# Performance work log

Measured on AMD Instinct MI355X. Metric: run time of the kernel, lower is better.

Reference implementation:

```python
import jax, jax.numpy as jnp
import numpy as np
from itertools import product

EPS = 1e-6
P = 3  # heatmap_size; corr channels = P**3 = 27


def l2_on_axis(x, axis=1):
    return jnp.sqrt(jnp.sum(x * x, axis=axis, keepdims=True) + EPS)


def reduce_masked_mean(x, mask):
    return jnp.sum(x * mask) / (jnp.sum(mask) + EPS)


def smoothl1(d):
    a = jnp.abs(d)
    return jnp.where(a < 1.0, 0.5 * d * d, a - 0.5)


def corr3d(f0, f1):
    # 3D correlation volume, patch P^3, zero padding. (B,C,D,H,W)->(B,P^3,D,H,W)
    B, C, D, H, W = f0.shape
    pad = P // 2
    f1p = jnp.pad(f1, ((0, 0), (0, 0), (pad, pad), (pad, pad), (pad, pad)))
    outs = []
    for dz in range(P):
        for dy in range(P):
            for dx in range(P):
                s = f1p[:, :, dz:dz + D, dy:dy + H, dx:dx + W]
                outs.append(jnp.einsum('bcdhw,bcdhw->bdhw', f0, s))
    return jnp.stack(outs, axis=1)


def flow_head(cc, W1, b1, W2, b2):
    cc = jax.nn.relu(cc)
    cc = cc / (jnp.sqrt(jnp.sum(cc * cc, axis=1, keepdims=True)) + EPS)  # l2_normalize dim=1
    h = jnp.einsum('oc,bcdhw->bodhw', W1, cc) + b1[None, :, None, None, None]
    h = jnp.where(h > 0, h, 0.01 * h)  # LeakyReLU
    return jnp.einsum('oc,bcdhw->bodhw', W2, h) + b2[None, :, None, None, None]


def backwarp(feat, flow):
    # trilinear backwarp, zero padding outside; flow ch: (dx->W, dy->H, dz->D)
    B, C, D, H, W = feat.shape
    zz, yy, xx = jnp.meshgrid(jnp.arange(D, dtype=flow.dtype),
                              jnp.arange(H, dtype=flow.dtype),
                              jnp.arange(W, dtype=flow.dtype), indexing='ij')
    xs = xx[None] + flow[:, 0]
    ys = yy[None] + flow[:, 1]
    zs = zz[None] + flow[:, 2]
    x0, y0, z0 = jnp.floor(xs), jnp.floor(ys), jnp.floor(zs)
    featf = feat.reshape(B, C, D * H * W)
    out = jnp.zeros_like(feat)
    for cz, cy, cx in product((0, 1), (0, 1), (0, 1)):
        zi, yi, xi = z0 + cz, y0 + cy, x0 + cx
        w = (1 - jnp.abs(zs - zi)) * (1 - jnp.abs(ys - yi)) * (1 - jnp.abs(xs - xi))
        valid = ((zi >= 0) & (zi < D) & (yi >= 0) & (yi < H) & (xi >= 0) & (xi < W)).astype(feat.dtype)
        idx = ((jnp.clip(zi, 0, D - 1) * H + jnp.clip(yi, 0, H - 1)) * W
               + jnp.clip(xi, 0, W - 1)).astype(jnp.int32).reshape(B, -1)
        g = jnp.take_along_axis(featf, idx[:, None, :], axis=2).reshape(B, C, D, H, W)
        out = out + g * (w * valid)[:, None]
    return out


def gradient3d_abs(x):
    dz = jnp.abs(jnp.pad(x[:, :, 1:] - x[:, :, :-1], ((0, 0), (0, 0), (0, 1), (0, 0), (0, 0))))
    dy = jnp.abs(jnp.pad(x[:, :, :, 1:] - x[:, :, :, :-1], ((0, 0), (0, 0), (0, 0), (0, 1), (0, 0))))
    dx = jnp.abs(jnp.pad(x[:, :, :, :, 1:] - x[:, :, :, :, :-1], ((0, 0), (0, 0), (0, 0), (0, 0), (0, 1))))
    return dx, dy, dz


def setup_inputs() -> dict:
    key = jax.random.key(0)
    ks = jax.random.split(key, 8)
    B, C, D, H, W = 2, 32, 64, 64, 64
    return {
        'feat0': jax.random.normal(ks[0], (B, C, D, H, W), jnp.float32),
        'feat1': jax.random.normal(ks[1], (B, C, D, H, W), jnp.float32),
        'flow_g': jax.random.normal(ks[2], (B, 3, D, H, W), jnp.float32),
        'mask_g': jax.random.uniform(ks[3], (B, 1, D, H, W), jnp.float32),
        'W1': jax.random.normal(ks[4], (64, P ** 3), jnp.float32) * 0.05,
        'b1': jnp.zeros((64,), jnp.float32),
        'W2': jax.random.normal(ks[5], (3, 64), jnp.float32) * 0.05,
        'b2': jnp.zeros((3,), jnp.float32),
        'is_synth': 0,
    }


def reference(feat0, feat1, flow_g, mask_g, W1, b1, W2, b2, is_synth):
    B, C, D, H, W = feat0.shape
    # hinge loss (feat1_aligned == feat1 at iteration 0)
    hinge_vox = jax.nn.relu(0.2 - l2_on_axis(feat1 - feat0))
    hinge_mask = (jnp.sum(jnp.abs(flow_g), axis=1, keepdims=True) > 1.0).astype(feat0.dtype)
    hinge_loss = reduce_masked_mean(hinge_vox, hinge_mask)

    # single scale sc=1.0
    flow_forw = flow_head(corr3d(feat0, feat1), W1, b1, W2, b2)
    flow_back = flow_head(corr3d(feat1, feat0), W1, b1, W2, b2)

    feat1_aligned = backwarp(feat1, flow_forw)
    ones1 = jnp.ones((B, 1, D, H, W), feat0.dtype)
    valid1 = backwarp(ones1, flow_forw)
    valid0 = backwarp(ones1, flow_forw)  # faithful: source also uses flow_total_forw

    feat_diff = reduce_masked_mean(l2_on_axis(feat1_aligned - feat0), valid1 * valid0)
    warp_loss_cumu = feat_diff  # * sc (=1)

    l1_diff = jnp.mean(smoothl1(flow_forw - flow_g), axis=1, keepdims=True)
    l2_diff = jnp.mean((flow_forw - flow_g) ** 2, axis=1, keepdims=True)
    nonzero = (jnp.sum(jnp.abs(flow_g), axis=1, keepdims=True) > 0.01).astype(feat0.dtype) * mask_g
    yeszero = (1.0 - nonzero) * mask_g
    l1_bal = 0.5 * (reduce_masked_mean(l1_diff, nonzero) + reduce_masked_mean(l1_diff, yeszero))
    l2_bal = 0.5 * (reduce_masked_mean(l2_diff, nonzero) + reduce_masked_mean(l2_diff, yeszero))

    fb_al = backwarp(flow_back, jax.lax.stop_gradient(flow_forw))
    ff_al = backwarp(flow_forw, jax.lax.stop_gradient(flow_back))
    cycle_loss = jnp.mean(smoothl1(flow_forw + fb_al)) + jnp.mean(smoothl1(flow_back + ff_al))

    dx, dy, dz = gradient3d_abs(flow_forw)
    smooth_forw = jnp.mean(dx + dy + dx, axis=1, keepdims=True)  # faithful: dx counted twice
    dx, dy, dz = gradient3d_abs(flow_back)
    smooth_back = jnp.mean(dx + dy + dx, axis=1, keepdims=True)
    smooth_loss = jnp.mean((smooth_forw + smooth_back) * 0.5)

    # all hyp coefficients = 1.0; is_synth selects identical coeffs here
    total_loss = hinge_loss + cycle_loss + l1_bal + l2_bal + warp_loss_cumu + smooth_loss
    return total_loss, flow_forw
```

## Files before the change

kernel.cpp:

```cpp
#include <hip/hip_runtime.h>
#include <math.h>

#define EPSF 1e-6f

typedef __attribute__((ext_vector_type(8))) short short8;
typedef __attribute__((ext_vector_type(4))) float f32x4;

constexpr int Bn = 2, Cn = 32, Dn = 64, Hn = 64, Wn = 64;
constexpr int HW  = Hn * Wn;
constexpr int DHW = Dn * HW;
constexpr int NVOX = Bn * DHW;


__device__ inline float sl1(float d) {
    float a = fabsf(d);
    return a < 1.f ? 0.5f * d * d : a - 0.5f;
}

__device__ inline int xcd_swz(int bid) {
    return (bid & 7) * 256 + (bid >> 3);
}

__device__ inline float dpp_left(float v) {
    int r = __builtin_amdgcn_update_dpp(0, __float_as_int(v), 0x138 ,
                                        0xF, 0xF, true);
    return __int_as_float(r);
}
__device__ inline float dpp_right(float v) {
    int r = __builtin_amdgcn_update_dpp(0, __float_as_int(v), 0x130 ,
                                        0xF, 0xF, true);
    return __int_as_float(r);
}

__device__ inline unsigned int bf16b(float f) {
    return (__float_as_uint(f) + 0x8000u) >> 16;
}
__device__ inline unsigned int bfpack(float lo, float hi) {
    return bf16b(lo) | ((__float_as_uint(hi) + 0x8000u) & 0xffff0000u);
}
__device__ inline float bf2f(unsigned short u) {
    return __uint_as_float((unsigned int)u << 16);
}

struct PairGather {
    int   pidx[4];
    int   sel[4];
    float w0[4], w1[4];
};

__device__ inline void warp_pair_setup(float flx, float fly, float flz,
                                       int x, int y, int z,
                                       PairGather& pg, float& wsum) {
    float xs = (float)x + flx, ys = (float)y + fly, zs = (float)z + flz;
    float xf = floorf(xs), yf = floorf(ys), zf = floorf(zs);
    float fx = xs - xf, fy = ys - yf, fz = zs - zf;
    int xi = (int)xf, yi = (int)yf, zi = (int)zf;

    int x0c = min(max(xi, 0), Wn - 1);
    bool xv0 = (xi >= 0) && (xi < Wn);
    bool xv1 = (xi + 1 >= 0) && (xi + 1 < Wn);
    int sel = (xi >= 0 && xi < Wn - 1) ? 1 : 0;
    float wx0 = xv0 ? (1.f - fx) : 0.f;
    float wx1 = xv1 ? fx : 0.f;

    wsum = 0.f;
#pragma unroll
    for (int cz = 0; cz < 2; cz++) {
        int zz = zi + cz;
        bool zv = (zz >= 0) && (zz < Dn);
        int zc = min(max(zz, 0), Dn - 1);
        float wz = (cz ? fz : 1.f - fz) * (zv ? 1.f : 0.f);
#pragma unroll
        for (int cy = 0; cy < 2; cy++) {
            int yy = yi + cy;
            bool yv = (yy >= 0) && (yy < Hn);
            int yc = min(max(yy, 0), Hn - 1);
            float wy = (cy ? fy : 1.f - fy) * (yv ? 1.f : 0.f);
            int k = cz * 2 + cy;
            int sp = (zc * Hn + yc) * Wn + x0c;
            pg.pidx[k] = min(sp, DHW - 2);
            pg.sel[k] = sel;
            float wzy = wz * wy;
            pg.w0[k] = wzy * wx0;
            pg.w1[k] = wzy * wx1;
            wsum += pg.w0[k] + pg.w1[k];
        }
    }
}

__device__ inline float gather8(const float* __restrict__ slab, const PairGather& pg) {
    float g = 0.f;
#pragma unroll
    for (int k = 0; k < 4; k++) {
        float2 v = *reinterpret_cast<const float2*>(slab + pg.pidx[k]);
        float second = pg.sel[k] ? v.y : v.x;
        g = fmaf(v.x, pg.w0[k], g);
        g = fmaf(second, pg.w1[k], g);
    }
    return g;
}

__global__ void prep_kernel(const float* __restrict__ W1, ushort* __restrict__ W1bf) {
    int i = blockIdx.x * 256 + threadIdx.x;
    if (i < 64 * 32) {
        int n = i >> 5, k = i & 31;
        float val = (k < 27) ? W1[n * 27 + k] : 0.f;
        W1bf[n * 40 + k] = (ushort)bf16b(val);
    }
}

__device__ __forceinline__ void flow_head_mfma(
        float* acc, ushort (&ccS)[4][64][40], int wid, int lane,
        const ushort* __restrict__ W1bf, const float* __restrict__ b1,
        const float* __restrict__ W2, const float* __restrict__ b2,
        float* __restrict__ flow_out, size_t fb0,
        float& mfx, float& mfy, float& mfz) {
    float ss = 0.f;
#pragma unroll
    for (int i = 0; i < 27; i++) {
        float r = acc[i] > 0.f ? acc[i] : 0.f;
        acc[i] = r;
        ss = fmaf(r, r, ss);
    }
    float inv = 1.0f / (sqrtf(ss) + EPSF);
#pragma unroll
    for (int i = 0; i < 27; i++) acc[i] *= inv;

    {
        unsigned int pk[16];
#pragma unroll
        for (int i = 0; i < 13; i++) pk[i] = bfpack(acc[2 * i], acc[2 * i + 1]);
        pk[13] = bfpack(acc[26], 0.f);
        pk[14] = 0u; pk[15] = 0u;
        uint2* rowp = reinterpret_cast<uint2*>(&ccS[wid][lane][0]);
#pragma unroll
        for (int i = 0; i < 8; i++) rowp[i] = make_uint2(pk[2 * i], pk[2 * i + 1]);
    }

    int c0 = lane & 15, oct = lane >> 4;

    short8 bfr[4];
#pragma unroll
    for (int t = 0; t < 4; t++)
        bfr[t] = *reinterpret_cast<const short8*>(W1bf + (size_t)(t * 16 + c0) * 40 + oct * 8);

    f32x4 b1v[4], w2f0[4], w2f1[4], w2f2[4];
#pragma unroll
    for (int mt = 0; mt < 4; mt++) {
        b1v[mt]  = *reinterpret_cast<const f32x4*>(b1 + mt * 16 + oct * 4);
        w2f0[mt] = *reinterpret_cast<const f32x4*>(W2 + mt * 16 + oct * 4);
        w2f1[mt] = *reinterpret_cast<const f32x4*>(W2 + 64 + mt * 16 + oct * 4);
        w2f2[mt] = *reinterpret_cast<const f32x4*>(W2 + 128 + mt * 16 + oct * 4);
    }
    float bb0 = b2[0], bb1 = b2[1], bb2 = b2[2];

#pragma unroll
    for (int nt = 0; nt < 4; nt++) {
        short8 afr = *reinterpret_cast<const short8*>(&ccS[wid][nt * 16 + c0][oct * 8]);
        f32x4 ac[4];
#pragma unroll
        for (int mt = 0; mt < 4; mt++) {
            f32x4 zero = {0.f, 0.f, 0.f, 0.f};
            ac[mt] = __builtin_amdgcn_mfma_f32_16x16x32_bf16(bfr[mt], afr, zero, 0, 0, 0);
        }
        float p0 = 0.f, p1 = 0.f, p2 = 0.f;
#pragma unroll
        for (int mt = 0; mt < 4; mt++) {
#pragma unroll
            for (int rg = 0; rg < 4; rg++) {
                float h = ac[mt][rg] + b1v[mt][rg];
                h = fmaxf(h, 0.01f * h);
                p0 = fmaf(w2f0[mt][rg], h, p0);
                p1 = fmaf(w2f1[mt][rg], h, p1);
                p2 = fmaf(w2f2[mt][rg], h, p2);
            }
        }
        p0 += __shfl_xor(p0, 16); p0 += __shfl_xor(p0, 32);
        p1 += __shfl_xor(p1, 16); p1 += __shfl_xor(p1, 32);
        p2 += __shfl_xor(p2, 16); p2 += __shfl_xor(p2, 32);
        if (oct == nt) {
            int vox = nt * 16 + c0;
            mfx = p0 + bb0; mfy = p1 + bb1; mfz = p2 + bb2;
            flow_out[fb0 + vox]           = mfx;
            flow_out[fb0 + DHW + vox]     = mfy;
            flow_out[fb0 + 2 * DHW + vox] = mfz;
        }
    }
}

__global__ __launch_bounds__(256)
void corr_fwd_kernel(const float* __restrict__ feat0, const float* __restrict__ feat1,
                     const ushort* __restrict__ W1bf, const float* __restrict__ b1,
                     const float* __restrict__ W2, const float* __restrict__ b2,
                     float* __restrict__ flow_forw,
                     const float* __restrict__ flow_g, const float* __restrict__ mask_g,
                     float* __restrict__ accum, ushort* __restrict__ craw) {
    __shared__ ushort ccS[4][64][40];

    int tid = threadIdx.x;
    int lane = tid & 63;
    int wid = __builtin_amdgcn_readfirstlane(tid >> 6);

    int R = xcd_swz(blockIdx.x) * 4 + wid;
    int y = R & 63, z = (R >> 6) & 63, b = R >> 12;

    const float* rp[9];
    float rmask[9];
    {
        int idx = 0;
#pragma unroll
        for (int dz = -1; dz <= 1; dz++) {
#pragma unroll
            for (int dy = -1; dy <= 1; dy++, idx++) {
                int zz = z + dz, yy = y + dy;
                bool valid = (zz >= 0) && (zz < Dn) && (yy >= 0) && (yy < Hn);
                int zc = min(max(zz, 0), Dn - 1);
                int yc = min(max(yy, 0), Hn - 1);
                rp[idx] = feat1 + (size_t)b * Cn * DHW + (size_t)zc * HW + (size_t)yc * Wn;
                rmask[idx] = valid ? 1.f : 0.f;
            }
        }
    }
    const float* ap = feat0 + (size_t)b * Cn * DHW + (size_t)z * HW + (size_t)y * Wn;

    float C[9], TL[9], TR[9];
#pragma unroll
    for (int r = 0; r < 9; r++) { C[r] = 0.f; TL[r] = 0.f; TR[r] = 0.f; }
    float diff2 = 0.f;

#pragma unroll 2
    for (int c = 0; c < Cn; c++) {
        float a = ap[lane];
        float rowv[9];
#pragma unroll
        for (int r = 0; r < 9; r++) rowv[r] = rp[r][lane];
        ap += DHW;
#pragma unroll
        for (int r = 0; r < 9; r++) rp[r] += DHW;

        float aL = dpp_left(a);
        float aR = dpp_right(a);
        float d = rowv[4] - a;
        diff2 = fmaf(d, d, diff2);
#pragma unroll
        for (int r = 0; r < 9; r++) {
            float rv = rowv[r];
            C[r]  = fmaf(a,  rv, C[r]);
            TL[r] = fmaf(aL, rv, TL[r]);
            TR[r] = fmaf(aR, rv, TR[r]);
        }
    }

    float acc[27];
#pragma unroll
    for (int r = 0; r < 9; r++) {
        acc[r * 3 + 0] = dpp_left(TR[r]) * rmask[r];
        acc[r * 3 + 1] = C[r] * rmask[r];
        acc[r * 3 + 2] = dpp_right(TL[r]) * rmask[r];
    }

    size_t vidx = (size_t)R * 64 + lane;
#pragma unroll
    for (int i = 0; i < 27; i++)
        craw[(size_t)i * NVOX + vidx] = (ushort)bf16b(acc[i]);

    size_t fb0 = (size_t)b * 3 * DHW + (size_t)z * HW + (size_t)y * Wn;
    float mfx, mfy, mfz;
    flow_head_mfma(acc, ccS, wid, lane, W1bf, b1, W2, b2, flow_forw, fb0,
                   mfx, mfy, mfz);

    size_t fbase = fb0 + lane;
    float gx = flow_g[fbase], gy = flow_g[fbase + DHW], gz = flow_g[fbase + 2 * DHW];
    float mg = mask_g[(size_t)b * DHW + (size_t)z * HW + y * Wn + lane];

    float ag = fabsf(gx) + fabsf(gy) + fabsf(gz);
    float hmask = ag > 1.0f ? 1.f : 0.f;
    float hv = 0.2f - sqrtf(diff2 + EPSF);
    hv = hv > 0.f ? hv : 0.f;

    float dx0 = mfx - gx, dy0 = mfy - gy, dz0 = mfz - gz;
    float l1 = (sl1(dx0) + sl1(dy0) + sl1(dz0)) * (1.f / 3.f);
    float l2 = (dx0 * dx0 + dy0 * dy0 + dz0 * dz0) * (1.f / 3.f);
    float nz = (ag > 0.01f ? 1.f : 0.f) * mg;
    float yz = (1.f - nz) * mg;

    PairGather pgF; float wsum;
    warp_pair_setup(mfx, mfy, mfz, lane, y, z, pgF, wsum);
    const float* f1b = feat1 + (size_t)b * Cn * DHW;
    const float* f0c = feat0 + (size_t)b * Cn * DHW + (size_t)z * HW + y * Wn + lane;
    float s = 0.f;
#pragma unroll 4
    for (int c = 0; c < Cn; c++) {
        float g = gather8(f1b + (size_t)c * DHW, pgF);
        float d = g - f0c[(size_t)c * DHW];
        s = fmaf(d, d, s);
    }
    float vm = wsum * wsum;
    float wnum = sqrtf(s + EPSF) * vm;

    float pv[10];
    pv[0] = hv * hmask; pv[1] = hmask;
    pv[2] = wnum;       pv[3] = vm;
    pv[4] = l1 * nz;    pv[5] = l1 * yz;
    pv[6] = l2 * nz;    pv[7] = l2 * yz;
    pv[8] = nz;         pv[9] = yz;

#pragma unroll
    for (int i = 0; i < 10; i++) {
        float val = pv[i];
        for (int off = 32; off; off >>= 1) val += __shfl_down(val, off, 64);
        pv[i] = val;
    }
    __shared__ float sred[10][4];
    if (lane == 0) {
#pragma unroll
        for (int i = 0; i < 10; i++) sred[i][wid] = pv[i];
    }
    __syncthreads();
    if (tid < 10) {
        atomicAdd(&accum[tid], sred[tid][0] + sred[tid][1] + sred[tid][2] + sred[tid][3]);
    }
}

__global__ __launch_bounds__(256)
void corr_bwd_kernel(const ushort* __restrict__ craw,
                     const ushort* __restrict__ W1bf, const float* __restrict__ b1,
                     const float* __restrict__ W2, const float* __restrict__ b2,
                     float* __restrict__ flow_back) {
    __shared__ ushort ccS[4][64][40];

    int tid = threadIdx.x;
    int lane = tid & 63;
    int wid = __builtin_amdgcn_readfirstlane(tid >> 6);

    int R = xcd_swz(blockIdx.x) * 4 + wid;
    int y = R & 63, z = (R >> 6) & 63, b = R >> 12;

    float acc[27];
#pragma unroll
    for (int sz = 0; sz < 3; sz++) {
#pragma unroll
        for (int sy = 0; sy < 3; sy++) {
            int zz = z + sz - 1, yy = y + sy - 1;
            bool valid = (zz >= 0) && (zz < Dn) && (yy >= 0) && (yy < Hn);
            int zc = min(max(zz, 0), Dn - 1);
            int yc = min(max(yy, 0), Hn - 1);
            float m = valid ? 1.f : 0.f;
            const ushort* rowb = craw + (size_t)b * DHW + (size_t)zc * HW + (size_t)yc * Wn + lane;
            int base = (sz * 3 + sy) * 3;
            float v0 = bf2f(rowb[(size_t)(26 - base) * NVOX]);
            float v1 = bf2f(rowb[(size_t)(25 - base) * NVOX]);
            float v2 = bf2f(rowb[(size_t)(24 - base) * NVOX]);
            acc[base + 0] = dpp_left(v0) * m;
            acc[base + 1] = v1 * m;
            acc[base + 2] = dpp_right(v2) * m;
        }
    }

    size_t fb0 = (size_t)b * 3 * DHW + (size_t)z * HW + (size_t)y * Wn;
    float mfx, mfy, mfz;
    flow_head_mfma(acc, ccS, wid, lane, W1bf, b1, W2, b2, flow_back, fb0,
                   mfx, mfy, mfz);
}

__global__ __launch_bounds__(256)
void slim_loss_kernel(const float* __restrict__ flowf, const float* __restrict__ flowb,
                      float* __restrict__ accum) {
    int tid = threadIdx.x;
    int v = xcd_swz(blockIdx.x) * 256 + tid;
    int x = v & 63, y = (v >> 6) & 63, z = (v >> 12) & 63, b = v >> 18;

    size_t sp = (size_t)z * HW + y * Wn + x;
    size_t f3 = (size_t)b * 3 * DHW + sp;

    float ffx = flowf[f3], ffy = flowf[f3 + DHW], ffz = flowf[f3 + 2 * DHW];
    float fbx = flowb[f3], fby = flowb[f3 + DHW], fbz = flowb[f3 + 2 * DHW];

    PairGather pgF; float wsumF;
    warp_pair_setup(ffx, ffy, ffz, x, y, z, pgF, wsumF);
    const float* fb_b = flowb + (size_t)b * 3 * DHW;
    float fbalx = gather8(fb_b, pgF);
    float fbaly = gather8(fb_b + DHW, pgF);
    float fbalz = gather8(fb_b + 2 * DHW, pgF);
    float cyc1 = sl1(ffx + fbalx) + sl1(ffy + fbaly) + sl1(ffz + fbalz);

    PairGather pgB; float wsumB;
    warp_pair_setup(fbx, fby, fbz, x, y, z, pgB, wsumB);
    const float* ff_b = flowf + (size_t)b * 3 * DHW;
    float ffalx = gather8(ff_b, pgB);
    float ffaly = gather8(ff_b + DHW, pgB);
    float ffalz = gather8(ff_b + 2 * DHW, pgB);
    float cyc2 = sl1(fbx + ffalx) + sl1(fby + ffaly) + sl1(fbz + ffalz);

    float sf = 0.f, sb2v = 0.f;
#pragma unroll
    for (int j = 0; j < 3; j++) {
        const float* pf = flowf + f3 + (size_t)j * DHW;
        float c0 = pf[0];
        float ddx = (x < Wn - 1) ? fabsf(pf[1] - c0) : 0.f;
        float ddy = (y < Hn - 1) ? fabsf(pf[Wn] - c0) : 0.f;
        sf += 2.f * ddx + ddy;
        const float* pb = flowb + f3 + (size_t)j * DHW;
        float c1 = pb[0];
        float ddx2 = (x < Wn - 1) ? fabsf(pb[1] - c1) : 0.f;
        float ddy2 = (y < Hn - 1) ? fabsf(pb[Wn] - c1) : 0.f;
        sb2v += 2.f * ddx2 + ddy2;
    }
    float smoothv = 0.5f * (sf * (1.f / 3.f) + sb2v * (1.f / 3.f));

    float pv[3] = { cyc1, cyc2, smoothv };
#pragma unroll
    for (int i = 0; i < 3; i++) {
        float val = pv[i];
        for (int off = 32; off; off >>= 1) val += __shfl_down(val, off, 64);
        pv[i] = val;
    }
    __shared__ float sred[3][4];
    int lane = tid & 63, wid = tid >> 6;
    if (lane == 0) {
#pragma unroll
        for (int i = 0; i < 3; i++) sred[i][wid] = pv[i];
    }
    __syncthreads();
    if (tid < 3) {
        atomicAdd(&accum[10 + tid], sred[tid][0] + sred[tid][1] + sred[tid][2] + sred[tid][3]);
    }
}

__global__ void finalize_kernel(const float* __restrict__ accum, float* __restrict__ out) {
    float hinge = accum[0] / (accum[1] + EPSF);
    float warp  = accum[2] / (accum[3] + EPSF);
    float l1b = 0.5f * (accum[4] / (accum[8] + EPSF) + accum[5] / (accum[9] + EPSF));
    float l2b = 0.5f * (accum[6] / (accum[8] + EPSF) + accum[7] / (accum[9] + EPSF));
    float n3 = 3.0f * (float)NVOX;
    float cyc = accum[10] / n3 + accum[11] / n3;
    float sm  = accum[12] / (float)NVOX;
    out[0] = hinge + cyc + l1b + l2b + warp + sm;
}

extern "C" void kernel_launch(void* const* d_in, const int* in_sizes, int n_in,
                              void* d_out, int out_size, void* d_ws, size_t ws_size,
                              hipStream_t stream) {
    const float* feat0  = (const float*)d_in[0];
    const float* feat1  = (const float*)d_in[1];
    const float* flow_g = (const float*)d_in[2];
    const float* mask_g = (const float*)d_in[3];
    const float* W1     = (const float*)d_in[4];
    const float* b1     = (const float*)d_in[5];
    const float* W2     = (const float*)d_in[6];
    const float* b2     = (const float*)d_in[7];

    float* out = (float*)d_out;
    float* accum = (float*)d_ws;
    ushort* W1bf = (ushort*)((char*)d_ws + 128);
    const size_t FLOWB_OFF = 8192;
    const size_t FLOWB_BYTES = (size_t)Bn * 3 * DHW * sizeof(float);
    float* flow_back = (float*)((char*)d_ws + FLOWB_OFF);
    const size_t CRAW_OFF = FLOWB_OFF + FLOWB_BYTES;
    ushort* craw = (ushort*)((char*)d_ws + CRAW_OFF);
    float* flow_forw = out + 1;

    hipMemsetAsync(d_ws, 0, 64, stream);

    dim3 block(256);
    prep_kernel<<<dim3(8), block, 0, stream>>>(W1, W1bf);

    corr_fwd_kernel<<<dim3(NVOX / 256), block, 0, stream>>>(
        feat0, feat1, W1bf, b1, W2, b2, flow_forw, flow_g, mask_g, accum, craw);
    corr_bwd_kernel<<<dim3(NVOX / 256), block, 0, stream>>>(
        craw, W1bf, b1, W2, b2, flow_back);
    slim_loss_kernel<<<dim3(NVOX / 256), block, 0, stream>>>(flow_forw, flow_back, accum);
    finalize_kernel<<<1, 1, 0, stream>>>(accum, out);
}
```

Measured before the change: 164.8 us.

## Process both batch elements per wave in forward correlation kernel

Each wave in the forward correlation kernel now handles the same (z,y) row for both batch items. It keeps two sets of 27 accumulators, runs the flow head twice, and does the warp-loss gathers for both batches in one loop. The grid is halved and the XCD swizzle chunk is adjusted to match. The aim is more independent loads and FMAs in flight per wave, plus shared address setup and fewer reductions and atomics. The cost is roughly twice the register use, which can lower occupancy or cause spills, and half as many blocks to fill the GPU.

```diff
diff --git a/kernel.cpp b/kernel.cpp
--- a/kernel.cpp
+++ b/kernel.cpp
@@ -10,6 +10,7 @@
 constexpr int HW  = Hn * Wn;
 constexpr int DHW = Dn * HW;
 constexpr int NVOX = Bn * DHW;
+constexpr size_t BS = (size_t)Cn * DHW;
 
 
 __device__ inline float sl1(float d) {
@@ -17,8 +18,8 @@
     return a < 1.f ? 0.5f * d * d : a - 0.5f;
 }
 
-__device__ inline int xcd_swz(int bid) {
-    return (bid & 7) * 256 + (bid >> 3);
+__device__ inline int xcd_swz(int bid, int chunk) {
+    return (bid & 7) * chunk + (bid >> 3);
 }
 
 __device__ inline float dpp_left(float v) {
@@ -201,10 +202,10 @@
     int lane = tid & 63;
     int wid = __builtin_amdgcn_readfirstlane(tid >> 6);
 
-    int R = xcd_swz(blockIdx.x) * 4 + wid;
-    int y = R & 63, z = (R >> 6) & 63, b = R >> 12;
-
-    const float* rp[9];
+    int R = xcd_swz(blockIdx.x, 128) * 4 + wid;
+    int y = R & 63, z = R >> 6;
+
+    const float* rp0[9];
     float rmask[9];
     {
         int idx = 0;
@@ -216,94 +217,124 @@
                 bool valid = (zz >= 0) && (zz < Dn) && (yy >= 0) && (yy < Hn);
                 int zc = min(max(zz, 0), Dn - 1);
                 int yc = min(max(yy, 0), Hn - 1);
-                rp[idx] = feat1 + (size_t)b * Cn * DHW + (size_t)zc * HW + (size_t)yc * Wn;
+                rp0[idx] = feat1 + (size_t)zc * HW + (size_t)yc * Wn;
                 rmask[idx] = valid ? 1.f : 0.f;
             }
         }
     }
-    const float* ap = feat0 + (size_t)b * Cn * DHW + (size_t)z * HW + (size_t)y * Wn;
-
-    float C[9], TL[9], TR[9];
-#pragma unroll
-    for (int r = 0; r < 9; r++) { C[r] = 0.f; TL[r] = 0.f; TR[r] = 0.f; }
-    float diff2 = 0.f;
+    const float* ap0 = feat0 + (size_t)z * HW + (size_t)y * Wn;
+
+    float C0[9], TL0[9], TR0[9], C1[9], TL1[9], TR1[9];
+#pragma unroll
+    for (int r = 0; r < 9; r++) {
+        C0[r] = 0.f; TL0[r] = 0.f; TR0[r] = 0.f;
+        C1[r] = 0.f; TL1[r] = 0.f; TR1[r] = 0.f;
+    }
+    float diff2_0 = 0.f, diff2_1 = 0.f;
 
 #pragma unroll 2
     for (int c = 0; c < Cn; c++) {
-        float a = ap[lane];
-        float rowv[9];
-#pragma unroll
-        for (int r = 0; r < 9; r++) rowv[r] = rp[r][lane];
-        ap += DHW;
-#pragma unroll
-        for (int r = 0; r < 9; r++) rp[r] += DHW;
-
-        float aL = dpp_left(a);
-        float aR = dpp_right(a);
-        float d = rowv[4] - a;
-        diff2 = fmaf(d, d, diff2);
+        float a0 = ap0[lane];
+        float a1 = ap0[lane + BS];
+        float rv0[9], rv1[9];
 #pragma unroll
         for (int r = 0; r < 9; r++) {
-            float rv = rowv[r];
-            C[r]  = fmaf(a,  rv, C[r]);
-            TL[r] = fmaf(aL, rv, TL[r]);
-            TR[r] = fmaf(aR, rv, TR[r]);
-        }
-    }
-
-    float acc[27];
-#pragma unroll
-    for (int r = 0; r < 9; r++) {
-        acc[r * 3 + 0] = dpp_left(TR[r]) * rmask[r];
-        acc[r * 3 + 1] = C[r] * rmask[r];
-        acc[r * 3 + 2] = dpp_right(TL[r]) * rmask[r];
-    }
-
-    size_t vidx = (size_t)R * 64 + lane;
-#pragma unroll
-    for (int i = 0; i < 27; i++)
-        craw[(size_t)i * NVOX + vidx] = (ushort)bf16b(acc[i]);
-
-    size_t fb0 = (size_t)b * 3 * DHW + (size_t)z * HW + (size_t)y * Wn;
-    float mfx, mfy, mfz;
-    flow_head_mfma(acc, ccS, wid, lane, W1bf, b1, W2, b2, flow_forw, fb0,
-                   mfx, mfy, mfz);
-
-    size_t fbase = fb0 + lane;
-    float gx = flow_g[fbase], gy = flow_g[fbase + DHW], gz = flow_g[fbase + 2 * DHW];
-    float mg = mask_g[(size_t)b * DHW + (size_t)z * HW + y * Wn + lane];
-
-    float ag = fabsf(gx) + fabsf(gy) + fabsf(gz);
-    float hmask = ag > 1.0f ? 1.f : 0.f;
-    float hv = 0.2f - sqrtf(diff2 + EPSF);
-    hv = hv > 0.f ? hv : 0.f;
-
-    float dx0 = mfx - gx, dy0 = mfy - gy, dz0 = mfz - gz;
-    float l1 = (sl1(dx0) + sl1(dy0) + sl1(dz0)) * (1.f / 3.f);
-    float l2 = (dx0 * dx0 + dy0 * dy0 + dz0 * dz0) * (1.f / 3.f);
-    float nz = (ag > 0.01f ? 1.f : 0.f) * mg;
-    float yz = (1.f - nz) * mg;
-
-    PairGather pgF; float wsum;
-    warp_pair_setup(mfx, mfy, mfz, lane, y, z, pgF, wsum);
-    const float* f1b = feat1 + (size_t)b * Cn * DHW;
-    const float* f0c = feat0 + (size_t)b * Cn * DHW + (size_t)z * HW + y * Wn + lane;
-    float s = 0.f;
+            rv0[r] = rp0[r][lane];
+            rv1[r] = rp0[r][lane + BS];
+        }
+        ap0 += DHW;
+#pragma unroll
+        for (int r = 0; r < 9; r++) rp0[r] += DHW;
+
+        float aL0 = dpp_left(a0), aR0 = dpp_right(a0);
+        float aL1 = dpp_left(a1), aR1 = dpp_right(a1);
+        float d0 = rv0[4] - a0; diff2_0 = fmaf(d0, d0, diff2_0);
+        float d1 = rv1[4] - a1; diff2_1 = fmaf(d1, d1, diff2_1);
+#pragma unroll
+        for (int r = 0; r < 9; r++) {
+            float v0 = rv0[r], v1 = rv1[r];
+            C0[r]  = fmaf(a0,  v0, C0[r]);
+            TL0[r] = fmaf(aL0, v0, TL0[r]);
+            TR0[r] = fmaf(aR0, v0, TR0[r]);
+            C1[r]  = fmaf(a1,  v1, C1[r]);
+            TL1[r] = fmaf(aL1, v1, TL1[r]);
+            TR1[r] = fmaf(aR1, v1, TR1[r]);
+        }
+    }
+
+    float mf[2][3];
+    float pv[10];
+#pragma unroll
+    for (int i = 0; i < 10; i++) pv[i] = 0.f;
+
+#pragma unroll
+    for (int j = 0; j < 2; j++) {
+        float acc[27];
+#pragma unroll
+        for (int r = 0; r < 9; r++) {
+            float m = rmask[r];
+            if (j == 0) {
+                acc[r * 3 + 0] = dpp_left(TR0[r]) * m;
+                acc[r * 3 + 1] = C0[r] * m;
+                acc[r * 3 + 2] = dpp_right(TL0[r]) * m;
+            } else {
+                acc[r * 3 + 0] = dpp_left(TR1[r]) * m;
+                acc[r * 3 + 1] = C1[r] * m;
+                acc[r * 3 + 2] = dpp_right(TL1[r]) * m;
+            }
+        }
+
+        size_t vidx = (size_t)(R + j * 4096) * 64 + lane;
+#pragma unroll
+        for (int i = 0; i < 27; i++)
+            craw[(size_t)i * NVOX + vidx] = (ushort)bf16b(acc[i]);
+
+        size_t fb0 = (size_t)j * 3 * DHW + (size_t)z * HW + (size_t)y * Wn;
+        flow_head_mfma(acc, ccS, wid, lane, W1bf, b1, W2, b2, flow_forw, fb0,
+                       mf[j][0], mf[j][1], mf[j][2]);
+
+        size_t fbase = fb0 + lane;
+        float gx = flow_g[fbase], gy = flow_g[fbase + DHW], gz = flow_g[fbase + 2 * DHW];
+        float mg = mask_g[(size_t)j * DHW + (size_t)z * HW + (size_t)y * Wn + lane];
+
+        float ag = fabsf(gx) + fabsf(gy) + fabsf(gz);
+        float hmask = ag > 1.0f ? 1.f : 0.f;
+        float dd2 = j == 0 ? diff2_0 : diff2_1;
+        float hv = 0.2f - sqrtf(dd2 + EPSF);
+        hv = hv > 0.f ? hv : 0.f;
+
+        float dx0 = mf[j][0] - gx, dy0 = mf[j][1] - gy, dz0 = mf[j][2] - gz;
+        float l1 = (sl1(dx0) + sl1(dy0) + sl1(dz0)) * (1.f / 3.f);
+        float l2 = (dx0 * dx0 + dy0 * dy0 + dz0 * dz0) * (1.f / 3.f);
+        float nz = (ag > 0.01f ? 1.f : 0.f) * mg;
+        float yz = (1.f - nz) * mg;
+
+        pv[0] += hv * hmask; pv[1] += hmask;
+        pv[4] += l1 * nz;    pv[5] += l1 * yz;
+        pv[6] += l2 * nz;    pv[7] += l2 * yz;
+        pv[8] += nz;         pv[9] += yz;
+    }
+
+    {
+        PairGather pg0, pg1; float ws0, ws1;
+        warp_pair_setup(mf[0][0], mf[0][1], mf[0][2], lane, y, z, pg0, ws0);
+        warp_pair_setup(mf[1][0], mf[1][1], mf[1][2], lane, y, z, pg1, ws1);
+        const float* f1b0 = feat1;
+        const float* f0c0 = feat0 + (size_t)z * HW + (size_t)y * Wn + lane;
+        float s0 = 0.f, s1 = 0.f;
 #pragma unroll 4
-    for (int c = 0; c < Cn; c++) {
-        float g = gather8(f1b + (size_t)c * DHW, pgF);
-        float d = g - f0c[(size_t)c * DHW];
-        s = fmaf(d, d, s);
-    }
-    float vm = wsum * wsum;
-    float wnum = sqrtf(s + EPSF) * vm;
-
-    float pv[10];
-    pv[0] = hv * hmask; pv[1] = hmask;
-    pv[2] = wnum;       pv[3] = vm;
-    pv[4] = l1 * nz;    pv[5] = l1 * yz;
-    pv[6] = l2 * nz;    pv[7] = l2 * yz;
-    pv[8] = nz;         pv[9] = yz;
+        for (int c = 0; c < Cn; c++) {
+            float g0 = gather8(f1b0 + (size_t)c * DHW, pg0);
+            float g1 = gather8(f1b0 + BS + (size_t)c * DHW, pg1);
+            float d0 = g0 - f0c0[(size_t)c * DHW];
+            float d1 = g1 - f0c0[BS + (size_t)c * DHW];
+            s0 = fmaf(d0, d0, s0);
+            s1 = fmaf(d1, d1, s1);
+        }
+        float vm0 = ws0 * ws0, vm1 = ws1 * ws1;
+        pv[2] = sqrtf(s0 + EPSF) * vm0 + sqrtf(s1 + EPSF) * vm1;
+        pv[3] = vm0 + vm1;
+    }
 
 #pragma unroll
     for (int i = 0; i < 10; i++) {
@@ -333,7 +364,7 @@
     int lane = tid & 63;
     int wid = __builtin_amdgcn_readfirstlane(tid >> 6);
 
-    int R = xcd_swz(blockIdx.x) * 4 + wid;
+    int R = xcd_swz(blockIdx.x, 256) * 4 + wid;
     int y = R & 63, z = (R >> 6) & 63, b = R >> 12;
 
     float acc[27];
@@ -367,7 +398,7 @@
 void slim_loss_kernel(const float* __restrict__ flowf, const float* __restrict__ flowb,
                       float* __restrict__ accum) {
     int tid = threadIdx.x;
-    int v = xcd_swz(blockIdx.x) * 256 + tid;
+    int v = xcd_swz(blockIdx.x, 256) * 256 + tid;
     int x = v & 63, y = (v >> 6) & 63, z = (v >> 12) & 63, b = v >> 18;
 
     size_t sp = (size_t)z * HW + y * Wn + x;
@@ -465,7 +496,7 @@
     dim3 block(256);
     prep_kernel<<<dim3(8), block, 0, stream>>>(W1, W1bf);
 
-    corr_fwd_kernel<<<dim3(NVOX / 256), block, 0, stream>>>(
+    corr_fwd_kernel<<<dim3(NVOX / 512), block, 0, stream>>>(
         feat0, feat1, W1bf, b1, W2, b2, flow_forw, flow_g, mask_g, accum, craw);
     corr_bwd_kernel<<<dim3(NVOX / 256), block, 0, stream>>>(
         craw, W1bf, b1, W2, b2, flow_back);
```

New measurement: 163.5 us. Within noise of the previous version (-0.8%).

## Stage shared feat1 neighbor rows in LDS with double buffering across waves

Applied to the files above, without the earlier changes.

The four waves in a block cover four consecutive y rows, and their 3x3 neighborhoods overlap. The correlation kernel now loads the 18 distinct feat1 rows per channel cooperatively into double-buffered LDS, prefetching the next channel into registers while the current one is computed. Each wave then reads its 9 rows from LDS instead of issuing 9 global loads per channel, cutting redundant global and cache traffic. The cost is a block-wide barrier every channel iteration, the LDS buffer being aliased with the flow-head staging area, and the loop no longer being unrolled.

```diff
diff --git a/kernel.cpp b/kernel.cpp
--- a/kernel.cpp
+++ b/kernel.cpp
@@ -10,6 +10,7 @@
 constexpr int HW  = Hn * Wn;
 constexpr int DHW = Dn * HW;
 constexpr int NVOX = Bn * DHW;
+constexpr size_t BS = (size_t)Cn * DHW;
 
 
 __device__ inline float sl1(float d) {
@@ -17,8 +18,8 @@
     return a < 1.f ? 0.5f * d * d : a - 0.5f;
 }
 
-__device__ inline int xcd_swz(int bid) {
-    return (bid & 7) * 256 + (bid >> 3);
+__device__ inline int xcd_swz(int bid, int chunk) {
+    return (bid & 7) * chunk + (bid >> 3);
 }
 
 __device__ inline float dpp_left(float v) {
@@ -110,7 +111,7 @@
 }
 
 __device__ __forceinline__ void flow_head_mfma(
-        float* acc, ushort (&ccS)[4][64][40], int wid, int lane,
+        float* acc, ushort (*ccS)[64][40], int wid, int lane,
         const ushort* __restrict__ W1bf, const float* __restrict__ b1,
         const float* __restrict__ W2, const float* __restrict__ b2,
         float* __restrict__ flow_out, size_t fb0,
@@ -195,16 +196,18 @@
                      float* __restrict__ flow_forw,
                      const float* __restrict__ flow_g, const float* __restrict__ mask_g,
                      float* __restrict__ accum, ushort* __restrict__ craw) {
-    __shared__ ushort ccS[4][64][40];
+    __shared__ __align__(16) char smem[4 * 64 * 40 * 2];
+    float (*sfeat)[18][64] = reinterpret_cast<float(*)[18][64]>(smem);
+    ushort (*ccS)[64][40]  = reinterpret_cast<ushort(*)[64][40]>(smem);
 
     int tid = threadIdx.x;
     int lane = tid & 63;
     int wid = __builtin_amdgcn_readfirstlane(tid >> 6);
 
-    int R = xcd_swz(blockIdx.x) * 4 + wid;
+    int R = xcd_swz(blockIdx.x, 256) * 4 + wid;
     int y = R & 63, z = (R >> 6) & 63, b = R >> 12;
-
-    const float* rp[9];
+    int y0 = y & ~3;
+
     float rmask[9];
     {
         int idx = 0;
@@ -213,33 +216,60 @@
 #pragma unroll
             for (int dy = -1; dy <= 1; dy++, idx++) {
                 int zz = z + dz, yy = y + dy;
-                bool valid = (zz >= 0) && (zz < Dn) && (yy >= 0) && (yy < Hn);
-                int zc = min(max(zz, 0), Dn - 1);
-                int yc = min(max(yy, 0), Hn - 1);
-                rp[idx] = feat1 + (size_t)b * Cn * DHW + (size_t)zc * HW + (size_t)yc * Wn;
-                rmask[idx] = valid ? 1.f : 0.f;
+                rmask[idx] = ((zz >= 0) && (zz < Dn) && (yy >= 0) && (yy < Hn)) ? 1.f : 0.f;
             }
         }
     }
-    const float* ap = feat0 + (size_t)b * Cn * DHW + (size_t)z * HW + (size_t)y * Wn;
+
+    const float* srp[5];
+#pragma unroll
+    for (int p = 0; p < 5; p++) {
+        int row = p * 4 + wid;
+        if (row < 18) {
+            int zc = min(max(z + row / 6 - 1, 0), Dn - 1);
+            int yc = min(max(y0 + row % 6 - 1, 0), Hn - 1);
+            srp[p] = feat1 + (size_t)b * BS + (size_t)zc * HW + (size_t)yc * Wn;
+        } else srp[p] = feat1;
+    }
+    const float* ap = feat0 + (size_t)b * BS + (size_t)z * HW + (size_t)y * Wn;
 
     float C[9], TL[9], TR[9];
 #pragma unroll
     for (int r = 0; r < 9; r++) { C[r] = 0.f; TL[r] = 0.f; TR[r] = 0.f; }
     float diff2 = 0.f;
 
-#pragma unroll 2
+#pragma unroll
+    for (int p = 0; p < 5; p++)
+        if (p * 4 + wid < 18)
+            sfeat[0][p * 4 + wid][lane] = srp[p][lane];
+    __syncthreads();
+
+#pragma unroll 1
     for (int c = 0; c < Cn; c++) {
+        int buf = c & 1;
         float a = ap[lane];
+        ap += DHW;
+
+        float stg[5];
+        if (c + 1 < Cn) {
+#pragma unroll
+            for (int p = 0; p < 5; p++)
+                if (p * 4 + wid < 18) { srp[p] += DHW; stg[p] = srp[p][lane]; }
+        }
+
         float rowv[9];
 #pragma unroll
-        for (int r = 0; r < 9; r++) rowv[r] = rp[r][lane];
-        ap += DHW;
-#pragma unroll
-        for (int r = 0; r < 9; r++) rp[r] += DHW;
-
-        float aL = dpp_left(a);
-        float aR = dpp_right(a);
+        for (int r = 0; r < 9; r++)
+            rowv[r] = sfeat[buf][(r / 3) * 6 + wid + (r % 3)][lane];
+
+        if (c + 1 < Cn) {
+#pragma unroll
+            for (int p = 0; p < 5; p++)
+                if (p * 4 + wid < 18)
+                    sfeat[buf ^ 1][p * 4 + wid][lane] = stg[p];
+        }
+
+        float aL = dpp_left(a), aR = dpp_right(a);
         float d = rowv[4] - a;
         diff2 = fmaf(d, d, diff2);
 #pragma unroll
@@ -249,6 +279,7 @@
             TL[r] = fmaf(aL, rv, TL[r]);
             TR[r] = fmaf(aR, rv, TR[r]);
         }
+        __syncthreads();
     }
 
     float acc[27];
@@ -286,8 +317,8 @@
 
     PairGather pgF; float wsum;
     warp_pair_setup(mfx, mfy, mfz, lane, y, z, pgF, wsum);
-    const float* f1b = feat1 + (size_t)b * Cn * DHW;
-    const float* f0c = feat0 + (size_t)b * Cn * DHW + (size_t)z * HW + y * Wn + lane;
+    const float* f1b = feat1 + (size_t)b * BS;
+    const float* f0c = feat0 + (size_t)b * BS + (size_t)z * HW + y * Wn + lane;
     float s = 0.f;
 #pragma unroll 4
     for (int c = 0; c < Cn; c++) {
@@ -327,13 +358,13 @@
                      const ushort* __restrict__ W1bf, const float* __restrict__ b1,
                      const float* __restrict__ W2, const float* __restrict__ b2,
                      float* __restrict__ flow_back) {
-    __shared__ ushort ccS[4][64][40];
+    __shared__ ushort ccSb[4][64][40];
 
     int tid = threadIdx.x;
     int lane = tid & 63;
     int wid = __builtin_amdgcn_readfirstlane(tid >> 6);
 
-    int R = xcd_swz(blockIdx.x) * 4 + wid;
+    int R = xcd_swz(blockIdx.x, 256) * 4 + wid;
     int y = R & 63, z = (R >> 6) & 63, b = R >> 12;
 
     float acc[27];
@@ -359,7 +390,7 @@
 
     size_t fb0 = (size_t)b * 3 * DHW + (size_t)z * HW + (size_t)y * Wn;
     float mfx, mfy, mfz;
-    flow_head_mfma(acc, ccS, wid, lane, W1bf, b1, W2, b2, flow_back, fb0,
+    flow_head_mfma(acc, ccSb, wid, lane, W1bf, b1, W2, b2, flow_back, fb0,
                    mfx, mfy, mfz);
 }
 
@@ -367,7 +398,7 @@
 void slim_loss_kernel(const float* __restrict__ flowf, const float* __restrict__ flowb,
                       float* __restrict__ accum) {
     int tid = threadIdx.x;
-    int v = xcd_swz(blockIdx.x) * 256 + tid;
+    int v = xcd_swz(blockIdx.x, 256) * 256 + tid;
     int x = v & 63, y = (v >> 6) & 63, z = (v >> 12) & 63, b = v >> 18;
 
     size_t sp = (size_t)z * HW + y * Wn + x;
```

After: 191.3 us. +16.0%, slower.

## Process two rows per wave in forward correlation with float2 loads and paired voxels

Applied to the files above, without the earlier changes.

The forward correlation kernel now assigns two y-rows to each wave. Each lane loads float2 pairs of adjacent x voxels and computes the shifted correlations for both voxels from registers, so only the half-wave boundary lanes need DPP shuffles. Block size drops to 128 threads with two waves, and the MFMA flow head and loss tail run twice per wave, once per row. Register use roughly doubles for the accumulators (six arrays of nine), which risks lower occupancy or spills.

```diff
diff --git a/kernel.cpp b/kernel.cpp
--- a/kernel.cpp
+++ b/kernel.cpp
@@ -10,6 +10,7 @@
 constexpr int HW  = Hn * Wn;
 constexpr int DHW = Dn * HW;
 constexpr int NVOX = Bn * DHW;
+constexpr size_t BS = (size_t)Cn * DHW;
 
 
 __device__ inline float sl1(float d) {
@@ -17,18 +18,16 @@
     return a < 1.f ? 0.5f * d * d : a - 0.5f;
 }
 
-__device__ inline int xcd_swz(int bid) {
-    return (bid & 7) * 256 + (bid >> 3);
+__device__ inline int xcd_swz(int bid, int chunk) {
+    return (bid & 7) * chunk + (bid >> 3);
 }
 
 __device__ inline float dpp_left(float v) {
-    int r = __builtin_amdgcn_update_dpp(0, __float_as_int(v), 0x138 ,
-                                        0xF, 0xF, true);
+    int r = __builtin_amdgcn_update_dpp(0, __float_as_int(v), 0x138, 0xF, 0xF, true);
     return __int_as_float(r);
 }
 __device__ inline float dpp_right(float v) {
-    int r = __builtin_amdgcn_update_dpp(0, __float_as_int(v), 0x130 ,
-                                        0xF, 0xF, true);
+    int r = __builtin_amdgcn_update_dpp(0, __float_as_int(v), 0x130, 0xF, 0xF, true);
     return __int_as_float(r);
 }
 
@@ -109,34 +108,12 @@
     }
 }
 
-__device__ __forceinline__ void flow_head_mfma(
-        float* acc, ushort (&ccS)[4][64][40], int wid, int lane,
+__device__ __forceinline__ void mfma_row(
+        ushort (*ccW)[40], int lane,
         const ushort* __restrict__ W1bf, const float* __restrict__ b1,
         const float* __restrict__ W2, const float* __restrict__ b2,
         float* __restrict__ flow_out, size_t fb0,
         float& mfx, float& mfy, float& mfz) {
-    float ss = 0.f;
-#pragma unroll
-    for (int i = 0; i < 27; i++) {
-        float r = acc[i] > 0.f ? acc[i] : 0.f;
-        acc[i] = r;
-        ss = fmaf(r, r, ss);
-    }
-    float inv = 1.0f / (sqrtf(ss) + EPSF);
-#pragma unroll
-    for (int i = 0; i < 27; i++) acc[i] *= inv;
-
-    {
-        unsigned int pk[16];
-#pragma unroll
-        for (int i = 0; i < 13; i++) pk[i] = bfpack(acc[2 * i], acc[2 * i + 1]);
-        pk[13] = bfpack(acc[26], 0.f);
-        pk[14] = 0u; pk[15] = 0u;
-        uint2* rowp = reinterpret_cast<uint2*>(&ccS[wid][lane][0]);
-#pragma unroll
-        for (int i = 0; i < 8; i++) rowp[i] = make_uint2(pk[2 * i], pk[2 * i + 1]);
-    }
-
     int c0 = lane & 15, oct = lane >> 4;
 
     short8 bfr[4];
@@ -156,7 +133,7 @@
 
 #pragma unroll
     for (int nt = 0; nt < 4; nt++) {
-        short8 afr = *reinterpret_cast<const short8*>(&ccS[wid][nt * 16 + c0][oct * 8]);
+        short8 afr = *reinterpret_cast<const short8*>(&ccW[nt * 16 + c0][oct * 8]);
         f32x4 ac[4];
 #pragma unroll
         for (int mt = 0; mt < 4; mt++) {
@@ -188,122 +165,208 @@
     }
 }
 
-__global__ __launch_bounds__(256)
+__device__ __forceinline__ void flow_head_mfma(
+        float* acc, ushort (*ccW)[40], int lane,
+        const ushort* __restrict__ W1bf, const float* __restrict__ b1,
+        const float* __restrict__ W2, const float* __restrict__ b2,
+        float* __restrict__ flow_out, size_t fb0,
+        float& mfx, float& mfy, float& mfz) {
+    float ss = 0.f;
+#pragma unroll
+    for (int i = 0; i < 27; i++) {
+        float r = acc[i] > 0.f ? acc[i] : 0.f;
+        acc[i] = r;
+        ss = fmaf(r, r, ss);
+    }
+    float inv = 1.0f / (sqrtf(ss) + EPSF);
+#pragma unroll
+    for (int i = 0; i < 27; i++) acc[i] *= inv;
+    {
+        unsigned int pk[16];
+#pragma unroll
+        for (int i = 0; i < 13; i++) pk[i] = bfpack(acc[2 * i], acc[2 * i + 1]);
+        pk[13] = bfpack(acc[26], 0.f);
+        pk[14] = 0u; pk[15] = 0u;
+        uint2* rowp = reinterpret_cast<uint2*>(&ccW[lane][0]);
+#pragma unroll
+        for (int i = 0; i < 8; i++) rowp[i] = make_uint2(pk[2 * i], pk[2 * i + 1]);
+    }
+    mfma_row(ccW, lane, W1bf, b1, W2, b2, flow_out, fb0, mfx, mfy, mfz);
+}
+
+__global__ __launch_bounds__(128)
 void corr_fwd_kernel(const float* __restrict__ feat0, const float* __restrict__ feat1,
                      const ushort* __restrict__ W1bf, const float* __restrict__ b1,
                      const float* __restrict__ W2, const float* __restrict__ b2,
                      float* __restrict__ flow_forw,
                      const float* __restrict__ flow_g, const float* __restrict__ mask_g,
                      float* __restrict__ accum, ushort* __restrict__ craw) {
-    __shared__ ushort ccS[4][64][40];
+    __shared__ ushort ccS[2][64][40];
+    __shared__ float sred[10][2];
 
     int tid = threadIdx.x;
     int lane = tid & 63;
     int wid = __builtin_amdgcn_readfirstlane(tid >> 6);
-
-    int R = xcd_swz(blockIdx.x) * 4 + wid;
-    int y = R & 63, z = (R >> 6) & 63, b = R >> 12;
-
-    const float* rp[9];
-    float rmask[9];
+    int xl = lane & 31, half = lane >> 5;
+
+    int P = xcd_swz(blockIdx.x, 256) * 2 + wid;
+    int Rb = P * 2;
+    int y0 = Rb & 63, z = (Rb >> 6) & 63, b = Rb >> 12;
+    int yh = y0 + half;
+
+    float mlo = (lane == 32) ? 0.f : 1.f;
+    float mhi = (lane == 31) ? 0.f : 1.f;
+
+    const float* zb0; const float* zb1; const float* zb2;
+    float rmaskv[9];
+    int voff[9];
     {
-        int idx = 0;
-#pragma unroll
-        for (int dz = -1; dz <= 1; dz++) {
-#pragma unroll
-            for (int dy = -1; dy <= 1; dy++, idx++) {
-                int zz = z + dz, yy = y + dy;
-                bool valid = (zz >= 0) && (zz < Dn) && (yy >= 0) && (yy < Hn);
-                int zc = min(max(zz, 0), Dn - 1);
+        const float* fb = feat1 + (size_t)b * BS;
+#pragma unroll
+        for (int dzi = 0; dzi < 3; dzi++) {
+            int zz = z + dzi - 1;
+            int zc = min(max(zz, 0), Dn - 1);
+            const float* zp = fb + (size_t)zc * HW;
+            if (dzi == 0) zb0 = zp; else if (dzi == 1) zb1 = zp; else zb2 = zp;
+            bool zv = (zz >= 0) && (zz < Dn);
+#pragma unroll
+            for (int dyi = 0; dyi < 3; dyi++) {
+                int yy = yh + dyi - 1;
                 int yc = min(max(yy, 0), Hn - 1);
-                rp[idx] = feat1 + (size_t)b * Cn * DHW + (size_t)zc * HW + (size_t)yc * Wn;
-                rmask[idx] = valid ? 1.f : 0.f;
+                voff[dzi * 3 + dyi] = yc * Wn + 2 * xl;
+                rmaskv[dzi * 3 + dyi] = (zv && yy >= 0 && yy < Hn) ? 1.f : 0.f;
             }
         }
     }
-    const float* ap = feat0 + (size_t)b * Cn * DHW + (size_t)z * HW + (size_t)y * Wn;
-
-    float C[9], TL[9], TR[9];
-#pragma unroll
-    for (int r = 0; r < 9; r++) { C[r] = 0.f; TL[r] = 0.f; TR[r] = 0.f; }
-    float diff2 = 0.f;
+    const float* ap = feat0 + (size_t)b * BS + (size_t)z * HW;
+    int offa = yh * Wn + 2 * xl;
+
+    float C0[9], C1[9], TL0[9], TL1[9], TR0[9], TR1[9];
+#pragma unroll
+    for (int r = 0; r < 9; r++) {
+        C0[r] = 0.f; C1[r] = 0.f; TL0[r] = 0.f;
+        TL1[r] = 0.f; TR0[r] = 0.f; TR1[r] = 0.f;
+    }
+    float d20 = 0.f, d21 = 0.f;
 
 #pragma unroll 2
     for (int c = 0; c < Cn; c++) {
-        float a = ap[lane];
-        float rowv[9];
-#pragma unroll
-        for (int r = 0; r < 9; r++) rowv[r] = rp[r][lane];
-        ap += DHW;
-#pragma unroll
-        for (int r = 0; r < 9; r++) rp[r] += DHW;
-
-        float aL = dpp_left(a);
-        float aR = dpp_right(a);
-        float d = rowv[4] - a;
-        diff2 = fmaf(d, d, diff2);
+        float2 a = *reinterpret_cast<const float2*>(ap + offa);
+        float2 rv[9];
+#pragma unroll
+        for (int j = 0; j < 9; j++) {
+            const float* base = (j < 3) ? zb0 : ((j < 6) ? zb1 : zb2);
+            rv[j] = *reinterpret_cast<const float2*>(base + voff[j]);
+        }
+        ap += DHW; zb0 += DHW; zb1 += DHW; zb2 += DHW;
+
+        float aL0 = dpp_left(a.y) * mlo;
+        float aR1 = dpp_right(a.x) * mhi;
+        float d0 = rv[4].x - a.x; d20 = fmaf(d0, d0, d20);
+        float d1 = rv[4].y - a.y; d21 = fmaf(d1, d1, d21);
 #pragma unroll
         for (int r = 0; r < 9; r++) {
-            float rv = rowv[r];
-            C[r]  = fmaf(a,  rv, C[r]);
-            TL[r] = fmaf(aL, rv, TL[r]);
-            TR[r] = fmaf(aR, rv, TR[r]);
-        }
-    }
-
-    float acc[27];
+            float vx = rv[r].x, vy = rv[r].y;
+            C0[r]  = fmaf(a.x, vx, C0[r]);
+            C1[r]  = fmaf(a.y, vy, C1[r]);
+            TL0[r] = fmaf(aL0, vx, TL0[r]);
+            TL1[r] = fmaf(a.x, vy, TL1[r]);
+            TR0[r] = fmaf(a.y, vx, TR0[r]);
+            TR1[r] = fmaf(aR1, vy, TR1[r]);
+        }
+    }
+
+    float acc0[27], acc1[27];
 #pragma unroll
     for (int r = 0; r < 9; r++) {
-        acc[r * 3 + 0] = dpp_left(TR[r]) * rmask[r];
-        acc[r * 3 + 1] = C[r] * rmask[r];
-        acc[r * 3 + 2] = dpp_right(TL[r]) * rmask[r];
-    }
-
-    size_t vidx = (size_t)R * 64 + lane;
-#pragma unroll
-    for (int i = 0; i < 27; i++)
-        craw[(size_t)i * NVOX + vidx] = (ushort)bf16b(acc[i]);
-
-    size_t fb0 = (size_t)b * 3 * DHW + (size_t)z * HW + (size_t)y * Wn;
-    float mfx, mfy, mfz;
-    flow_head_mfma(acc, ccS, wid, lane, W1bf, b1, W2, b2, flow_forw, fb0,
-                   mfx, mfy, mfz);
-
-    size_t fbase = fb0 + lane;
-    float gx = flow_g[fbase], gy = flow_g[fbase + DHW], gz = flow_g[fbase + 2 * DHW];
-    float mg = mask_g[(size_t)b * DHW + (size_t)z * HW + y * Wn + lane];
-
-    float ag = fabsf(gx) + fabsf(gy) + fabsf(gz);
-    float hmask = ag > 1.0f ? 1.f : 0.f;
-    float hv = 0.2f - sqrtf(diff2 + EPSF);
-    hv = hv > 0.f ? hv : 0.f;
-
-    float dx0 = mfx - gx, dy0 = mfy - gy, dz0 = mfz - gz;
-    float l1 = (sl1(dx0) + sl1(dy0) + sl1(dz0)) * (1.f / 3.f);
-    float l2 = (dx0 * dx0 + dy0 * dy0 + dz0 * dz0) * (1.f / 3.f);
-    float nz = (ag > 0.01f ? 1.f : 0.f) * mg;
-    float yz = (1.f - nz) * mg;
-
-    PairGather pgF; float wsum;
-    warp_pair_setup(mfx, mfy, mfz, lane, y, z, pgF, wsum);
-    const float* f1b = feat1 + (size_t)b * Cn * DHW;
-    const float* f0c = feat0 + (size_t)b * Cn * DHW + (size_t)z * HW + y * Wn + lane;
-    float s = 0.f;
+        float m = rmaskv[r];
+        acc0[r * 3 + 0] = dpp_left(TR1[r]) * mlo * m;
+        acc1[r * 3 + 0] = TR0[r] * m;
+        acc0[r * 3 + 1] = C0[r] * m;
+        acc1[r * 3 + 1] = C1[r] * m;
+        acc0[r * 3 + 2] = TL1[r] * m;
+        acc1[r * 3 + 2] = dpp_right(TL0[r]) * mhi * m;
+    }
+
+    {
+        size_t vbase = (size_t)b * DHW + (size_t)z * HW + (size_t)yh * Wn + 2 * xl;
+        unsigned int* cw = reinterpret_cast<unsigned int*>(craw);
+#pragma unroll
+        for (int i = 0; i < 27; i++)
+            cw[((size_t)i * NVOX + vbase) >> 1] = bfpack(acc0[i], acc1[i]);
+    }
+
+    float pv[10];
+#pragma unroll
+    for (int i = 0; i < 10; i++) pv[i] = 0.f;
+
+#pragma unroll 1
+    for (int r = 0; r < 2; r++) {
+        if (half == r) {
+#pragma unroll
+            for (int e = 0; e < 2; e++) {
+                float t[27]; float ss = 0.f;
+#pragma unroll
+                for (int i = 0; i < 27; i++) {
+                    float v = (e == 0) ? acc0[i] : acc1[i];
+                    v = v > 0.f ? v : 0.f;
+                    t[i] = v;
+                    ss = fmaf(v, v, ss);
+                }
+                float inv = 1.0f / (sqrtf(ss) + EPSF);
+                unsigned int pk[16];
+#pragma unroll
+                for (int i = 0; i < 13; i++) pk[i] = bfpack(t[2 * i] * inv, t[2 * i + 1] * inv);
+                pk[13] = bfpack(t[26] * inv, 0.f);
+                pk[14] = 0u; pk[15] = 0u;
+                uint2* rowp = reinterpret_cast<uint2*>(&ccS[wid][2 * xl + e][0]);
+#pragma unroll
+                for (int i = 0; i < 8; i++) rowp[i] = make_uint2(pk[2 * i], pk[2 * i + 1]);
+            }
+        }
+        int yr = y0 + r;
+        size_t fb0 = (size_t)b * 3 * DHW + (size_t)z * HW + (size_t)yr * Wn;
+        float mfx, mfy, mfz;
+        mfma_row(ccS[wid], lane, W1bf, b1, W2, b2, flow_forw, fb0, mfx, mfy, mfz);
+
+        int src = r * 32 + (lane >> 1);
+        float s0v = __shfl(d20, src, 64);
+        float s1v = __shfl(d21, src, 64);
+        float d2 = (lane & 1) ? s1v : s0v;
+
+        size_t fbase = fb0 + lane;
+        float gx = flow_g[fbase], gy = flow_g[fbase + DHW], gz = flow_g[fbase + 2 * DHW];
+        float mg = mask_g[(size_t)b * DHW + (size_t)z * HW + (size_t)yr * Wn + lane];
+
+        float ag = fabsf(gx) + fabsf(gy) + fabsf(gz);
+        float hmask = ag > 1.0f ? 1.f : 0.f;
+        float hv = 0.2f - sqrtf(d2 + EPSF);
+        hv = hv > 0.f ? hv : 0.f;
+
+        float dx0 = mfx - gx, dy0 = mfy - gy, dz0 = mfz - gz;
+        float l1 = (sl1(dx0) + sl1(dy0) + sl1(dz0)) * (1.f / 3.f);
+        float l2 = (dx0 * dx0 + dy0 * dy0 + dz0 * dz0) * (1.f / 3.f);
+        float nz = (ag > 0.01f ? 1.f : 0.f) * mg;
+        float yz = (1.f - nz) * mg;
+
+        PairGather pgF; float wsum;
+        warp_pair_setup(mfx, mfy, mfz, lane, yr, z, pgF, wsum);
+        const float* f1b = feat1 + (size_t)b * BS;
+        const float* f0c = feat0 + (size_t)b * BS + (size_t)z * HW + (size_t)yr * Wn + lane;
+        float s = 0.f;
 #pragma unroll 4
-    for (int c = 0; c < Cn; c++) {
-        float g = gather8(f1b + (size_t)c * DHW, pgF);
-        float d = g - f0c[(size_t)c * DHW];
-        s = fmaf(d, d, s);
-    }
-    float vm = wsum * wsum;
-    float wnum = sqrtf(s + EPSF) * vm;
-
-    float pv[10];
-    pv[0] = hv * hmask; pv[1] = hmask;
-    pv[2] = wnum;       pv[3] = vm;
-    pv[4] = l1 * nz;    pv[5] = l1 * yz;
-    pv[6] = l2 * nz;    pv[7] = l2 * yz;
-    pv[8] = nz;         pv[9] = yz;
+        for (int c = 0; c < Cn; c++) {
+            float g = gather8(f1b + (size_t)c * DHW, pgF);
+            float d = g - f0c[(size_t)c * DHW];
+            s = fmaf(d, d, s);
+        }
+        float vm = wsum * wsum;
+        pv[0] += hv * hmask; pv[1] += hmask;
+        pv[2] += sqrtf(s + EPSF) * vm; pv[3] += vm;
+        pv[4] += l1 * nz;    pv[5] += l1 * yz;
+        pv[6] += l2 * nz;    pv[7] += l2 * yz;
+        pv[8] += nz;         pv[9] += yz;
+    }
 
 #pragma unroll
     for (int i = 0; i < 10; i++) {
@@ -311,14 +374,13 @@
         for (int off = 32; off; off >>= 1) val += __shfl_down(val, off, 64);
         pv[i] = val;
     }
-    __shared__ float sred[10][4];
     if (lane == 0) {
 #pragma unroll
         for (int i = 0; i < 10; i++) sred[i][wid] = pv[i];
     }
     __syncthreads();
     if (tid < 10) {
-        atomicAdd(&accum[tid], sred[tid][0] + sred[tid][1] + sred[tid][2] + sred[tid][3]);
+        atomicAdd(&accum[tid], sred[tid][0] + sred[tid][1]);
     }
 }
 
@@ -327,13 +389,13 @@
                      const ushort* __restrict__ W1bf, const float* __restrict__ b1,
                      const float* __restrict__ W2, const float* __restrict__ b2,
                      float* __restrict__ flow_back) {
-    __shared__ ushort ccS[4][64][40];
+    __shared__ ushort ccSb[4][64][40];
 
     int tid = threadIdx.x;
     int lane = tid & 63;
     int wid = __builtin_amdgcn_readfirstlane(tid >> 6);
 
-    int R = xcd_swz(blockIdx.x) * 4 + wid;
+    int R = xcd_swz(blockIdx.x, 256) * 4 + wid;
     int y = R & 63, z = (R >> 6) & 63, b = R >> 12;
 
     float acc[27];
@@ -359,7 +421,7 @@
 
     size_t fb0 = (size_t)b * 3 * DHW + (size_t)z * HW + (size_t)y * Wn;
     float mfx, mfy, mfz;
-    flow_head_mfma(acc, ccS, wid, lane, W1bf, b1, W2, b2, flow_back, fb0,
+    flow_head_mfma(acc, ccSb[wid], lane, W1bf, b1, W2, b2, flow_back, fb0,
                    mfx, mfy, mfz);
 }
 
@@ -367,7 +429,7 @@
 void slim_loss_kernel(const float* __restrict__ flowf, const float* __restrict__ flowb,
                       float* __restrict__ accum) {
     int tid = threadIdx.x;
-    int v = xcd_swz(blockIdx.x) * 256 + tid;
+    int v = xcd_swz(blockIdx.x, 256) * 256 + tid;
     int x = v & 63, y = (v >> 6) & 63, z = (v >> 12) & 63, b = v >> 18;
 
     size_t sp = (size_t)z * HW + y * Wn + x;
@@ -462,13 +524,12 @@
 
     hipMemsetAsync(d_ws, 0, 64, stream);
 
-    dim3 block(256);
-    prep_kernel<<<dim3(8), block, 0, stream>>>(W1, W1bf);
-
-    corr_fwd_kernel<<<dim3(NVOX / 256), block, 0, stream>>>(
+    prep_kernel<<<dim3(8), dim3(256), 0, stream>>>(W1, W1bf);
+
+    corr_fwd_kernel<<<dim3(2048), dim3(128), 0, stream>>>(
         feat0, feat1, W1bf, b1, W2, b2, flow_forw, flow_g, mask_g, accum, craw);
-    corr_bwd_kernel<<<dim3(NVOX / 256), block, 0, stream>>>(
+    corr_bwd_kernel<<<dim3(NVOX / 256), dim3(256), 0, stream>>>(
         craw, W1bf, b1, W2, b2, flow_back);
-    slim_loss_kernel<<<dim3(NVOX / 256), block, 0, stream>>>(flow_forw, flow_back, accum);
+    slim_loss_kernel<<<dim3(NVOX / 256), dim3(256), 0, stream>>>(flow_forw, flow_back, accum);
     finalize_kernel<<<1, 1, 0, stream>>>(accum, out);
 }
```

Result: slower. 186.0 us (+12.9%).
